# Performance work log

Measured on AMD Instinct MI355X. Metric: run time of the kernel, lower is better.

## Reference

```python
import jax, jax.numpy as jnp
import numpy as np

EPS = 1e-5


def setup_inputs() -> dict:
    key = jax.random.key(0)
    ks = jax.random.split(key, 7)
    N, M, D, H, DM = 8192, 128, 64, 8, 1024  # tokens, num_memories, d_memory, heads, d_model
    return {
        "query": jax.random.normal(ks[0], (N, DM), dtype=jnp.float32),
        "addresses": jax.random.normal(ks[1], (M, D), dtype=jnp.float32),
        "memories": jax.random.normal(ks[2], (N, M, D), dtype=jnp.float32),
        "Wq": jax.random.normal(ks[3], (DM, H * D), dtype=jnp.float32) / np.sqrt(DM),
        "bq": jax.random.normal(ks[4], (H * D,), dtype=jnp.float32) * 0.01,
        "Wo": jax.random.normal(ks[5], (H * D, DM), dtype=jnp.float32) / np.sqrt(H * D),
        "bo": jax.random.normal(ks[6], (DM,), dtype=jnp.float32) * 0.01,
    }


def reference(query, addresses, memories, Wq, bq, Wo, bo):
    N = query.shape[0]
    M, D = addresses.shape
    # Query projection -> heads: (N, H, D)
    q = (query @ Wq + bq).reshape(N, -1, D)
    q = jax.nn.relu(q)  # kernel feature map on query
    # Keys: memory content + learned addresses, kernel feature map
    k = jax.nn.relu(memories + addresses)  # (N, M, D)
    # make_kernel: contract over the num_memories dim
    matrix = jnp.einsum("nmd,nme->nde", k, memories)  # (N, D, D)
    normalizer = jnp.sum(k, axis=-2)  # (N, D)
    # read_from_kernel
    numerator = jnp.einsum("nhd,nde->nhe", q, matrix)  # (N, H, D)
    denominator = jnp.einsum("nhd,nd->nh", q, normalizer)[..., None] + EPS
    attn = numerator / denominator  # (N, H, D)
    # merge heads back to d_model
    return attn.reshape(N, -1) @ Wo + bo
```

## Files before the change

### kernel.cpp

```cpp
#include <hip/hip_runtime.h>

typedef __bf16 bf16x8 __attribute__((ext_vector_type(8)));
typedef __bf16 bf16x4 __attribute__((ext_vector_type(4)));
typedef __bf16 bf16x2 __attribute__((ext_vector_type(2)));
typedef float  f32x4  __attribute__((ext_vector_type(4)));

__device__ __forceinline__ void gload_lds16(const void* g, void* l) {
    auto gp = reinterpret_cast<const __attribute__((address_space(1))) unsigned int*>(
        reinterpret_cast<uintptr_t>(g));
    auto lp = reinterpret_cast<__attribute__((address_space(3))) unsigned int*>(
        reinterpret_cast<uintptr_t>(l));
    __builtin_amdgcn_global_load_lds(gp, lp, 16, 0, 0);
}

__global__ __launch_bounds__(256) void convert_to_bf16(
    const float* __restrict__ src, __bf16* __restrict__ dst, int n8)
{
    const int i = blockIdx.x * 256 + threadIdx.x;
    if (i < n8) {
        f32x4 a = ((const f32x4*)src)[2 * i];
        f32x4 b = ((const f32x4*)src)[2 * i + 1];
        bf16x8 o;
        #pragma unroll
        for (int j = 0; j < 4; ++j) { o[j] = (__bf16)a[j]; o[4 + j] = (__bf16)b[j]; }
        ((bf16x8*)dst)[i] = o;
    }
}

__global__ __launch_bounds__(256) void transpose_to_bf16(
    const float* __restrict__ src, __bf16* __restrict__ dst, int R, int C)
{
    __shared__ float tile[32][33];
    const int tx = threadIdx.x & 31, ty = threadIdx.x >> 5;
    const int r0 = blockIdx.y * 32, c0 = blockIdx.x * 32;
    #pragma unroll
    for (int i = ty; i < 32; i += 8)
        tile[i][tx] = src[(size_t)(r0 + i) * C + c0 + tx];
    __syncthreads();
    #pragma unroll
    for (int i = ty; i < 32; i += 8)
        dst[(size_t)(c0 + i) * R + r0 + tx] = (__bf16)tile[tx][i];
}

template<bool RELU, bool OBF16>
__global__ __launch_bounds__(256) void gemm_lds(
    const __bf16* __restrict__ A, const __bf16* __restrict__ BT,
    const float* __restrict__ bias, void* __restrict__ Outp,
    int M, int N, int K)
{
    __shared__ __bf16 As[128][32];
    __shared__ __bf16 Bs[128][32];

    const int tid = threadIdx.x, lane = tid & 63, w = tid >> 6;
    const int wm = w >> 1, wn = w & 1;
    const int m0 = blockIdx.y * 128, n0 = blockIdx.x * 128;
    const int r = lane & 15, g = lane >> 4;

    const int srow = lane >> 2;
    const int scol = (lane & 3) * 8;
    const __bf16* gA = A  + (size_t)(m0 + 32 * w + srow) * K + scol;
    const __bf16* gB = BT + (size_t)(n0 + 32 * w + srow) * K + scol;

    f32x4 acc[4][4];
    const f32x4 zero = {0.f, 0.f, 0.f, 0.f};
    #pragma unroll
    for (int mi = 0; mi < 4; ++mi)
        #pragma unroll
        for (int ni = 0; ni < 4; ++ni) acc[mi][ni] = zero;

    for (int k0 = 0; k0 < K; k0 += 32) {
        __syncthreads();
        gload_lds16(gA + k0,          &As[32 * w][0]);
        gload_lds16(gA + 16 * K + k0, &As[32 * w + 16][0]);
        gload_lds16(gB + k0,          &Bs[32 * w][0]);
        gload_lds16(gB + 16 * K + k0, &Bs[32 * w + 16][0]);
        __syncthreads();

        bf16x8 af[4], bfr[4];
        #pragma unroll
        for (int mi = 0; mi < 4; ++mi)
            af[mi] = *(const bf16x8*)&As[wm * 64 + mi * 16 + r][g * 8];
        #pragma unroll
        for (int ni = 0; ni < 4; ++ni)
            bfr[ni] = *(const bf16x8*)&Bs[wn * 64 + ni * 16 + r][g * 8];
        #pragma unroll
        for (int mi = 0; mi < 4; ++mi)
            #pragma unroll
            for (int ni = 0; ni < 4; ++ni)
                acc[mi][ni] = __builtin_amdgcn_mfma_f32_16x16x32_bf16(
                    af[mi], bfr[ni], acc[mi][ni], 0, 0, 0);
    }

    const int orow = m0 + wm * 64 + g * 4;
    const int ocol = n0 + wn * 64 + r;
    #pragma unroll
    for (int ni = 0; ni < 4; ++ni) {
        const float bb = bias[ocol + ni * 16];
        #pragma unroll
        for (int mi = 0; mi < 4; ++mi) {
            #pragma unroll
            for (int q = 0; q < 4; ++q) {
                float v = acc[mi][ni][q] + bb;
                if constexpr (RELU) v = fmaxf(v, 0.f);
                const size_t o = (size_t)(orow + mi * 16 + q) * N + ocol + ni * 16;
                if constexpr (OBF16) ((__bf16*)Outp)[o] = (__bf16)v;
                else                 ((float*)Outp)[o]  = v;
            }
        }
    }
}

__device__ __forceinline__ int kbyte(int m, int e) {
    return m * 128 + ((((e >> 3) ^ (m & 7))) << 4) + (e & 7) * 2;
}

__global__ __launch_bounds__(256, 4) void memory_attn_mfma(
    const __bf16* __restrict__ Q,
    const float*  __restrict__ mem,
    const __bf16* __restrict__ adrb,
    __bf16* __restrict__ attn)
{
    __shared__ __align__(16) unsigned char kbuf[4][4096];
    __shared__ __align__(16) unsigned char tbuf[4][5120];
    __shared__ float denl[4][8];

    const int tid = threadIdx.x, lane = tid & 63, w = tid >> 6;
    const int n = blockIdx.x * 4 + w;
    const int v = lane & 15, g = lane >> 4;
    const int e4 = 4 * v;

    unsigned char* kb = kbuf[w];
    unsigned char* tb = tbuf[w];
    const float* pmem = mem + (size_t)n * 128 * 64;

    const __bf16* qp = Q + (size_t)n * 512 + v * 64 + 8 * g;
    const bf16x8 qf0 = *(const bf16x8*)(qp);
    const bf16x8 qf1 = *(const bf16x8*)(qp + 32);

    f32x4 acc[4];
    const f32x4 zero = {0.f, 0.f, 0.f, 0.f};
    #pragma unroll
    for (int nb = 0; nb < 4; ++nb) acc[nb] = zero;
    float psum = 0.f;

    f32x4 cm[8];
    #pragma unroll
    for (int i = 0; i < 4; ++i) {
        const int mo = 8 * i + 2 * g;
        cm[2 * i]     = *(const f32x4*)(pmem + (size_t)mo * 64 + e4);
        cm[2 * i + 1] = *(const f32x4*)(pmem + (size_t)(mo + 1) * 64 + e4);
    }

    #pragma unroll
    for (int c = 0; c < 4; ++c) {
        const int mb = c * 32;
        f32x4 nm[8];
        if (c < 3) {
            #pragma unroll
            for (int i = 0; i < 4; ++i) {
                const int mo = mb + 32 + 8 * i + 2 * g;
                nm[2 * i]     = *(const f32x4*)(pmem + (size_t)mo * 64 + e4);
                nm[2 * i + 1] = *(const f32x4*)(pmem + (size_t)(mo + 1) * 64 + e4);
            }
        }
        #pragma unroll
        for (int i = 0; i < 4; ++i) {
            const int mo = mb + 8 * i + 2 * g;
            const bf16x4 a0 = *(const bf16x4*)(adrb + (size_t)(mo & 127) * 64 + e4);
            const bf16x4 a1 = *(const bf16x4*)(adrb + (size_t)((mo + 1) & 127) * 64 + e4);
            const f32x4 m0 = cm[2 * i], m1 = cm[2 * i + 1];
            bf16x4 k0, k1;
            #pragma unroll
            for (int j = 0; j < 4; ++j) {
                k0[j] = (__bf16)fmaxf(m0[j] + (float)a0[j], 0.f);
                k1[j] = (__bf16)fmaxf(m1[j] + (float)a1[j], 0.f);
            }
            const int mo_l = mo & 31;
            *(bf16x4*)(kb + kbyte(mo_l,     e4)) = k0;
            *(bf16x4*)(kb + kbyte(mo_l + 1, e4)) = k1;
            const int kap = 8 * ((mo_l >> 2) & 3) + 4 * (mo_l >> 4) + (mo_l & 3);
            #pragma unroll
            for (int j2 = 0; j2 < 4; ++j2) {
                bf16x2 p = { (__bf16)m0[j2], (__bf16)m1[j2] };
                *(bf16x2*)(tb + (size_t)(e4 + j2) * 80 + kap * 2) = p;
            }
        }

        f32x4 sA0 = zero, sA1 = zero;
        {
            const bf16x8 a00 = *(const bf16x8*)(kb + kbyte(v,      8 * g));
            const bf16x8 a01 = *(const bf16x8*)(kb + kbyte(v,      32 + 8 * g));
            const bf16x8 a10 = *(const bf16x8*)(kb + kbyte(v + 16, 8 * g));
            const bf16x8 a11 = *(const bf16x8*)(kb + kbyte(v + 16, 32 + 8 * g));
            sA0 = __builtin_amdgcn_mfma_f32_16x16x32_bf16(a00, qf0, sA0, 0, 0, 0);
            sA0 = __builtin_amdgcn_mfma_f32_16x16x32_bf16(a01, qf1, sA0, 0, 0, 0);
            sA1 = __builtin_amdgcn_mfma_f32_16x16x32_bf16(a10, qf0, sA1, 0, 0, 0);
            sA1 = __builtin_amdgcn_mfma_f32_16x16x32_bf16(a11, qf1, sA1, 0, 0, 0);
        }
        psum += sA0[0] + sA0[1] + sA0[2] + sA0[3]
              + sA1[0] + sA1[1] + sA1[2] + sA1[3];

        bf16x8 pa;
        #pragma unroll
        for (int q = 0; q < 4; ++q) {
            pa[q]     = (__bf16)sA0[q];
            pa[4 + q] = (__bf16)sA1[q];
        }

        #pragma unroll
        for (int nb = 0; nb < 4; ++nb) {
            const bf16x8 bf = *(const bf16x8*)(tb + (size_t)(16 * nb + v) * 80 + 16 * g);
            acc[nb] = __builtin_amdgcn_mfma_f32_16x16x32_bf16(pa, bf, acc[nb], 0, 0, 0);
        }

        if (c < 3) {
            #pragma unroll
            for (int t = 0; t < 8; ++t) cm[t] = nm[t];
        }
    }

    psum += __shfl_xor(psum, 16);
    psum += __shfl_xor(psum, 32);
    if (lane < 8) denl[w][lane] = psum;

    if (g < 2) {
        const f32x4 d4 = *(const f32x4*)&denl[w][4 * g];
        float inv[4];
        #pragma unroll
        for (int q = 0; q < 4; ++q) inv[q] = 1.f / (d4[q] + 1e-5f);
        #pragma unroll
        for (int nb = 0; nb < 4; ++nb) {
            #pragma unroll
            for (int q = 0; q < 4; ++q) {
                attn[(size_t)n * 512 + (4 * g + q) * 64 + 16 * nb + v] =
                    (__bf16)(acc[nb][q] * inv[q]);
            }
        }
    }
}

extern "C" void kernel_launch(void* const* d_in, const int* in_sizes, int n_in,
                              void* d_out, int out_size, void* d_ws, size_t ws_size,
                              hipStream_t stream)
{
    const float* query     = (const float*)d_in[0];
    const float* addresses = (const float*)d_in[1];
    const float* memories  = (const float*)d_in[2];
    const float* Wq        = (const float*)d_in[3];
    const float* bq        = (const float*)d_in[4];
    const float* Wo        = (const float*)d_in[5];
    const float* bo        = (const float*)d_in[6];
    float* out = (float*)d_out;

    char* ws = (char*)d_ws;
    __bf16* WqT  = (__bf16*)(ws);
    __bf16* WoT  = (__bf16*)(ws + (1 << 20));
    __bf16* Qb   = (__bf16*)(ws + (2 << 20));
    __bf16* Ab   = (__bf16*)(ws + (10 << 20));
    __bf16* Adrb = (__bf16*)(ws + (18 << 20));
    __bf16* Qbf  = (__bf16*)d_out;

    convert_to_bf16<<<4096, 256, 0, stream>>>(query, Qbf, 8192 * 1024 / 8);
    convert_to_bf16<<<4, 256, 0, stream>>>(addresses, Adrb, 128 * 64 / 8);
    transpose_to_bf16<<<dim3(512 / 32, 1024 / 32), 256, 0, stream>>>(Wq, WqT, 1024, 512);
    transpose_to_bf16<<<dim3(1024 / 32, 512 / 32), 256, 0, stream>>>(Wo, WoT, 512, 1024);

    gemm_lds<true, true><<<dim3(512 / 128, 8192 / 128), 256, 0, stream>>>(
        Qbf, WqT, bq, Qb, 8192, 512, 1024);

    memory_attn_mfma<<<dim3(8192 / 4), 256, 0, stream>>>(Qb, memories, Adrb, Ab);

    gemm_lds<false, false><<<dim3(1024 / 128, 8192 / 128), 256, 0, stream>>>(
        Ab, WoT, bo, out, 8192, 1024, 512);
}
```

Baseline: 128.8 us.

## Retile Q-projection GEMM and remap memory loads in attention kernel

The GEMM gains a BN template parameter, and the query projection now uses 64-wide column tiles. This doubles its block count (256 to 512) so more compute units have work. In the memory-attention kernel, each lane now loads four consecutive memory rows instead of two interleaved pairs, which lets the transposed tile be written as bf16x4 rather than bf16x2. The occupancy hint drops from 4 to 3 blocks per CU, which gives the compiler more registers for the larger per-lane staging. The risks are lower occupancy and more redundant A-tile loads in the smaller-tile GEMM.

```diff
diff --git a/kernel.cpp b/kernel.cpp
--- a/kernel.cpp
+++ b/kernel.cpp
@@ -42,59 +42,61 @@
         dst[(size_t)(c0 + i) * R + r0 + tx] = (__bf16)tile[tx][i];
 }
 
-template<bool RELU, bool OBF16>
+template<int BN, bool RELU, bool OBF16>
 __global__ __launch_bounds__(256) void gemm_lds(
     const __bf16* __restrict__ A, const __bf16* __restrict__ BT,
     const float* __restrict__ bias, void* __restrict__ Outp,
     int M, int N, int K)
 {
+    constexpr int FN = BN / 32;
     __shared__ __bf16 As[128][32];
-    __shared__ __bf16 Bs[128][32];
+    __shared__ __bf16 Bs[BN][32];
 
     const int tid = threadIdx.x, lane = tid & 63, w = tid >> 6;
     const int wm = w >> 1, wn = w & 1;
-    const int m0 = blockIdx.y * 128, n0 = blockIdx.x * 128;
+    const int m0 = blockIdx.y * 128, n0 = blockIdx.x * BN;
     const int r = lane & 15, g = lane >> 4;
 
     const int srow = lane >> 2;
     const int scol = (lane & 3) * 8;
     const __bf16* gA = A  + (size_t)(m0 + 32 * w + srow) * K + scol;
-    const __bf16* gB = BT + (size_t)(n0 + 32 * w + srow) * K + scol;
-
-    f32x4 acc[4][4];
+    const __bf16* gB = BT + (size_t)(n0 + (BN / 4) * w + srow) * K + scol;
+
+    f32x4 acc[4][FN];
     const f32x4 zero = {0.f, 0.f, 0.f, 0.f};
     #pragma unroll
     for (int mi = 0; mi < 4; ++mi)
         #pragma unroll
-        for (int ni = 0; ni < 4; ++ni) acc[mi][ni] = zero;
+        for (int ni = 0; ni < FN; ++ni) acc[mi][ni] = zero;
 
     for (int k0 = 0; k0 < K; k0 += 32) {
         __syncthreads();
         gload_lds16(gA + k0,          &As[32 * w][0]);
         gload_lds16(gA + 16 * K + k0, &As[32 * w + 16][0]);
-        gload_lds16(gB + k0,          &Bs[32 * w][0]);
-        gload_lds16(gB + 16 * K + k0, &Bs[32 * w + 16][0]);
+        #pragma unroll
+        for (int t = 0; t < BN / 64; ++t)
+            gload_lds16(gB + (size_t)(16 * t) * K + k0, &Bs[(BN / 4) * w + 16 * t][0]);
         __syncthreads();
 
-        bf16x8 af[4], bfr[4];
+        bf16x8 af[4], bfr[FN];
         #pragma unroll
         for (int mi = 0; mi < 4; ++mi)
             af[mi] = *(const bf16x8*)&As[wm * 64 + mi * 16 + r][g * 8];
         #pragma unroll
-        for (int ni = 0; ni < 4; ++ni)
-            bfr[ni] = *(const bf16x8*)&Bs[wn * 64 + ni * 16 + r][g * 8];
+        for (int ni = 0; ni < FN; ++ni)
+            bfr[ni] = *(const bf16x8*)&Bs[wn * (FN * 16) + ni * 16 + r][g * 8];
         #pragma unroll
         for (int mi = 0; mi < 4; ++mi)
             #pragma unroll
-            for (int ni = 0; ni < 4; ++ni)
+            for (int ni = 0; ni < FN; ++ni)
                 acc[mi][ni] = __builtin_amdgcn_mfma_f32_16x16x32_bf16(
                     af[mi], bfr[ni], acc[mi][ni], 0, 0, 0);
     }
 
     const int orow = m0 + wm * 64 + g * 4;
-    const int ocol = n0 + wn * 64 + r;
-    #pragma unroll
-    for (int ni = 0; ni < 4; ++ni) {
+    const int ocol = n0 + wn * (FN * 16) + r;
+    #pragma unroll
+    for (int ni = 0; ni < FN; ++ni) {
         const float bb = bias[ocol + ni * 16];
         #pragma unroll
         for (int mi = 0; mi < 4; ++mi) {
@@ -114,7 +116,7 @@
     return m * 128 + ((((e >> 3) ^ (m & 7))) << 4) + (e & 7) * 2;
 }
 
-__global__ __launch_bounds__(256, 4) void memory_attn_mfma(
+__global__ __launch_bounds__(256, 3) void memory_attn_mfma(
     const __bf16* __restrict__ Q,
     const float*  __restrict__ mem,
     const __bf16* __restrict__ adrb,
@@ -127,7 +129,8 @@
     const int tid = threadIdx.x, lane = tid & 63, w = tid >> 6;
     const int n = blockIdx.x * 4 + w;
     const int v = lane & 15, g = lane >> 4;
-    const int e4 = 4 * v;
+    const int sv = lane >> 2, sg = lane & 3;
+    const int e4s = 4 * sv;
 
     unsigned char* kb = kbuf[w];
     unsigned char* tb = tbuf[w];
@@ -145,11 +148,10 @@
 
     f32x4 cm[8];
     #pragma unroll
-    for (int i = 0; i < 4; ++i) {
-        const int mo = 8 * i + 2 * g;
-        cm[2 * i]     = *(const f32x4*)(pmem + (size_t)mo * 64 + e4);
-        cm[2 * i + 1] = *(const f32x4*)(pmem + (size_t)(mo + 1) * 64 + e4);
-    }
+    for (int i = 0; i < 2; ++i)
+        #pragma unroll
+        for (int j = 0; j < 4; ++j)
+            cm[4 * i + j] = *(const f32x4*)(pmem + (size_t)(16 * i + 4 * sg + j) * 64 + e4s);
 
     #pragma unroll
     for (int c = 0; c < 4; ++c) {
@@ -157,32 +159,32 @@
         f32x4 nm[8];
         if (c < 3) {
             #pragma unroll
-            for (int i = 0; i < 4; ++i) {
-                const int mo = mb + 32 + 8 * i + 2 * g;
-                nm[2 * i]     = *(const f32x4*)(pmem + (size_t)mo * 64 + e4);
-                nm[2 * i + 1] = *(const f32x4*)(pmem + (size_t)(mo + 1) * 64 + e4);
-            }
-        }
-        #pragma unroll
-        for (int i = 0; i < 4; ++i) {
-            const int mo = mb + 8 * i + 2 * g;
-            const bf16x4 a0 = *(const bf16x4*)(adrb + (size_t)(mo & 127) * 64 + e4);
-            const bf16x4 a1 = *(const bf16x4*)(adrb + (size_t)((mo + 1) & 127) * 64 + e4);
-            const f32x4 m0 = cm[2 * i], m1 = cm[2 * i + 1];
-            bf16x4 k0, k1;
+            for (int i = 0; i < 2; ++i)
+                #pragma unroll
+                for (int j = 0; j < 4; ++j)
+                    nm[4 * i + j] = *(const f32x4*)(
+                        pmem + (size_t)(mb + 32 + 16 * i + 4 * sg + j) * 64 + e4s);
+        }
+        #pragma unroll
+        for (int i = 0; i < 2; ++i) {
+            const int mo_b = 16 * i + 4 * sg;
             #pragma unroll
             for (int j = 0; j < 4; ++j) {
-                k0[j] = (__bf16)fmaxf(m0[j] + (float)a0[j], 0.f);
-                k1[j] = (__bf16)fmaxf(m1[j] + (float)a1[j], 0.f);
-            }
-            const int mo_l = mo & 31;
-            *(bf16x4*)(kb + kbyte(mo_l,     e4)) = k0;
-            *(bf16x4*)(kb + kbyte(mo_l + 1, e4)) = k1;
-            const int kap = 8 * ((mo_l >> 2) & 3) + 4 * (mo_l >> 4) + (mo_l & 3);
-            #pragma unroll
-            for (int j2 = 0; j2 < 4; ++j2) {
-                bf16x2 p = { (__bf16)m0[j2], (__bf16)m1[j2] };
-                *(bf16x2*)(tb + (size_t)(e4 + j2) * 80 + kap * 2) = p;
+                const int mo = mo_b + j;
+                const bf16x4 av = *(const bf16x4*)(adrb + (size_t)(mb + mo) * 64 + e4s);
+                const f32x4 mv = cm[4 * i + j];
+                bf16x4 kv;
+                #pragma unroll
+                for (int t = 0; t < 4; ++t)
+                    kv[t] = (__bf16)fmaxf(mv[t] + (float)av[t], 0.f);
+                *(bf16x4*)(kb + kbyte(mo, e4s)) = kv;
+            }
+            const int kb2 = 16 * sg + 8 * i;
+            #pragma unroll
+            for (int t = 0; t < 4; ++t) {
+                bf16x4 p = { (__bf16)cm[4 * i + 0][t], (__bf16)cm[4 * i + 1][t],
+                             (__bf16)cm[4 * i + 2][t], (__bf16)cm[4 * i + 3][t] };
+                *(bf16x4*)(tb + (size_t)(e4s + t) * 80 + kb2) = p;
             }
         }
 
@@ -265,11 +267,11 @@
     transpose_to_bf16<<<dim3(512 / 32, 1024 / 32), 256, 0, stream>>>(Wq, WqT, 1024, 512);
     transpose_to_bf16<<<dim3(1024 / 32, 512 / 32), 256, 0, stream>>>(Wo, WoT, 512, 1024);
 
-    gemm_lds<true, true><<<dim3(512 / 128, 8192 / 128), 256, 0, stream>>>(
+    gemm_lds<64, true, true><<<dim3(512 / 64, 8192 / 128), 256, 0, stream>>>(
         Qbf, WqT, bq, Qb, 8192, 512, 1024);
 
     memory_attn_mfma<<<dim3(8192 / 4), 256, 0, stream>>>(Qb, memories, Adrb, Ab);
 
-    gemm_lds<false, false><<<dim3(1024 / 128, 8192 / 128), 256, 0, stream>>>(
+    gemm_lds<128, false, false><<<dim3(1024 / 128, 8192 / 128), 256, 0, stream>>>(
         Ab, WoT, bo, out, 8192, 1024, 512);
 }
```

After: 132.5 us. 1.03x slower.

## Fuse query bf16 conversion into Q-projection GEMM and merge prep kernels

Applied to the files above, without the earlier changes.

Removes the separate pass that converts the full fp32 query matrix to bf16 by having the Q-projection GEMM load fp32 tiles and convert them while staging into LDS, with a narrower 64-column tile to increase block count. The weight transposes and address conversion are merged into one launch to cut launch overhead. The memory-attention kernel drops its software prefetch of memories and its launch bounds, relying on the compiler and occupancy instead. The GEMM's fp32 A loads are now synchronous register loads rather than async LDS loads, and the query is re-read across eight column blocks instead of four.

```diff
diff --git a/kernel.cpp b/kernel.cpp
--- a/kernel.cpp
+++ b/kernel.cpp
@@ -13,39 +13,115 @@
     __builtin_amdgcn_global_load_lds(gp, lp, 16, 0, 0);
 }
 
-__global__ __launch_bounds__(256) void convert_to_bf16(
-    const float* __restrict__ src, __bf16* __restrict__ dst, int n8)
-{
-    const int i = blockIdx.x * 256 + threadIdx.x;
-    if (i < n8) {
-        f32x4 a = ((const f32x4*)src)[2 * i];
-        f32x4 b = ((const f32x4*)src)[2 * i + 1];
+__global__ __launch_bounds__(256) void prep_all(
+    const float* __restrict__ Wq, const float* __restrict__ Wo,
+    const float* __restrict__ adr,
+    __bf16* __restrict__ WqT, __bf16* __restrict__ WoT,
+    __bf16* __restrict__ adrb)
+{
+    __shared__ float tile[32][33];
+    const int bid = blockIdx.x, tid = threadIdx.x;
+
+    if (bid < 1024) {
+        const float* src; __bf16* dst; int R, C, r0, c0;
+        if (bid < 512) {
+            src = Wq; dst = WqT; R = 1024; C = 512;
+            c0 = (bid & 15) * 32; r0 = (bid >> 4) * 32;
+        } else {
+            const int b = bid - 512;
+            src = Wo; dst = WoT; R = 512; C = 1024;
+            c0 = (b & 31) * 32; r0 = (b >> 5) * 32;
+        }
+        const int tx = tid & 31, ty = tid >> 5;
+        #pragma unroll
+        for (int i = ty; i < 32; i += 8)
+            tile[i][tx] = src[(size_t)(r0 + i) * C + c0 + tx];
+        __syncthreads();
+        #pragma unroll
+        for (int i = ty; i < 32; i += 8)
+            dst[(size_t)(c0 + i) * R + r0 + tx] = (__bf16)tile[tx][i];
+    } else {
+        const int i = (bid - 1024) * 256 + tid;
+        f32x4 a = ((const f32x4*)adr)[2 * i];
+        f32x4 b = ((const f32x4*)adr)[2 * i + 1];
         bf16x8 o;
         #pragma unroll
         for (int j = 0; j < 4; ++j) { o[j] = (__bf16)a[j]; o[4 + j] = (__bf16)b[j]; }
-        ((bf16x8*)dst)[i] = o;
-    }
-}
-
-__global__ __launch_bounds__(256) void transpose_to_bf16(
-    const float* __restrict__ src, __bf16* __restrict__ dst, int R, int C)
-{
-    __shared__ float tile[32][33];
-    const int tx = threadIdx.x & 31, ty = threadIdx.x >> 5;
-    const int r0 = blockIdx.y * 32, c0 = blockIdx.x * 32;
-    #pragma unroll
-    for (int i = ty; i < 32; i += 8)
-        tile[i][tx] = src[(size_t)(r0 + i) * C + c0 + tx];
-    __syncthreads();
-    #pragma unroll
-    for (int i = ty; i < 32; i += 8)
-        dst[(size_t)(c0 + i) * R + r0 + tx] = (__bf16)tile[tx][i];
-}
-
-template<bool RELU, bool OBF16>
-__global__ __launch_bounds__(256) void gemm_lds(
+        ((bf16x8*)adrb)[i] = o;
+    }
+}
+
+__global__ __launch_bounds__(256) void gemm_qproj(
+    const float* __restrict__ A, const __bf16* __restrict__ BT,
+    const float* __restrict__ bias, __bf16* __restrict__ Out,
+    int M, int N, int K)
+{
+    __shared__ __bf16 As[128][40];
+    __shared__ __bf16 Bs[64][32];
+
+    const int tid = threadIdx.x, lane = tid & 63, w = tid >> 6;
+    const int wm = w >> 1, wn = w & 1;
+    const int m0 = blockIdx.y * 128, n0 = blockIdx.x * 64;
+    const int r = lane & 15, g = lane >> 4;
+
+    const __bf16* gB = BT + (size_t)(n0 + 16 * w + (lane >> 2)) * K + (lane & 3) * 8;
+
+    f32x4 acc[4][2];
+    const f32x4 zero = {0.f, 0.f, 0.f, 0.f};
+    #pragma unroll
+    for (int mi = 0; mi < 4; ++mi)
+        #pragma unroll
+        for (int ni = 0; ni < 2; ++ni) acc[mi][ni] = zero;
+
+    for (int k0 = 0; k0 < K; k0 += 32) {
+        __syncthreads();
+        gload_lds16(gB + k0, &Bs[16 * w][0]);
+        #pragma unroll
+        for (int i = 0; i < 4; ++i) {
+            const int idx = tid + i * 256;
+            const int row = idx >> 3, c4 = (idx & 7) * 4;
+            f32x4 v = *(const f32x4*)(A + (size_t)(m0 + row) * K + k0 + c4);
+            bf16x4 b;
+            b[0] = (__bf16)v[0]; b[1] = (__bf16)v[1];
+            b[2] = (__bf16)v[2]; b[3] = (__bf16)v[3];
+            *(bf16x4*)&As[row][c4] = b;
+        }
+        __syncthreads();
+
+        bf16x8 af[4], bfr[2];
+        #pragma unroll
+        for (int mi = 0; mi < 4; ++mi)
+            af[mi] = *(const bf16x8*)&As[wm * 64 + mi * 16 + r][g * 8];
+        #pragma unroll
+        for (int ni = 0; ni < 2; ++ni)
+            bfr[ni] = *(const bf16x8*)&Bs[wn * 32 + ni * 16 + r][g * 8];
+        #pragma unroll
+        for (int mi = 0; mi < 4; ++mi)
+            #pragma unroll
+            for (int ni = 0; ni < 2; ++ni)
+                acc[mi][ni] = __builtin_amdgcn_mfma_f32_16x16x32_bf16(
+                    af[mi], bfr[ni], acc[mi][ni], 0, 0, 0);
+    }
+
+    const int orow = m0 + wm * 64 + g * 4;
+    const int ocol = n0 + wn * 32 + r;
+    #pragma unroll
+    for (int ni = 0; ni < 2; ++ni) {
+        const float bb = bias[ocol + ni * 16];
+        #pragma unroll
+        for (int mi = 0; mi < 4; ++mi) {
+            #pragma unroll
+            for (int q = 0; q < 4; ++q) {
+                float v = fmaxf(acc[mi][ni][q] + bb, 0.f);
+                Out[(size_t)(orow + mi * 16 + q) * N + ocol + ni * 16] = (__bf16)v;
+            }
+        }
+    }
+}
+
+__global__ __launch_bounds__(256) void gemm_oproj(
     const __bf16* __restrict__ A, const __bf16* __restrict__ BT,
-    const float* __restrict__ bias, void* __restrict__ Outp,
+    const float* __restrict__ bias, float* __restrict__ Out,
     int M, int N, int K)
 {
     __shared__ __bf16 As[128][32];
@@ -100,11 +176,8 @@
         for (int mi = 0; mi < 4; ++mi) {
             #pragma unroll
             for (int q = 0; q < 4; ++q) {
-                float v = acc[mi][ni][q] + bb;
-                if constexpr (RELU) v = fmaxf(v, 0.f);
-                const size_t o = (size_t)(orow + mi * 16 + q) * N + ocol + ni * 16;
-                if constexpr (OBF16) ((__bf16*)Outp)[o] = (__bf16)v;
-                else                 ((float*)Outp)[o]  = v;
+                Out[(size_t)(orow + mi * 16 + q) * N + ocol + ni * 16]
+                    = acc[mi][ni][q] + bb;
             }
         }
     }
@@ -114,7 +187,7 @@
     return m * 128 + ((((e >> 3) ^ (m & 7))) << 4) + (e & 7) * 2;
 }
 
-__global__ __launch_bounds__(256, 4) void memory_attn_mfma(
+__global__ void memory_attn_mfma(
     const __bf16* __restrict__ Q,
     const float*  __restrict__ mem,
     const __bf16* __restrict__ adrb,
@@ -127,11 +200,9 @@
     const int tid = threadIdx.x, lane = tid & 63, w = tid >> 6;
     const int n = blockIdx.x * 4 + w;
     const int v = lane & 15, g = lane >> 4;
-    const int e4 = 4 * v;
 
     unsigned char* kb = kbuf[w];
     unsigned char* tb = tbuf[w];
-    const float* pmem = mem + (size_t)n * 128 * 64;
 
     const __bf16* qp = Q + (size_t)n * 512 + v * 64 + 8 * g;
     const bf16x8 qf0 = *(const bf16x8*)(qp);
@@ -143,46 +214,30 @@
     for (int nb = 0; nb < 4; ++nb) acc[nb] = zero;
     float psum = 0.f;
 
-    f32x4 cm[8];
-    #pragma unroll
-    for (int i = 0; i < 4; ++i) {
-        const int mo = 8 * i + 2 * g;
-        cm[2 * i]     = *(const f32x4*)(pmem + (size_t)mo * 64 + e4);
-        cm[2 * i + 1] = *(const f32x4*)(pmem + (size_t)(mo + 1) * 64 + e4);
-    }
-
-    #pragma unroll
     for (int c = 0; c < 4; ++c) {
         const int mb = c * 32;
-        f32x4 nm[8];
-        if (c < 3) {
-            #pragma unroll
-            for (int i = 0; i < 4; ++i) {
-                const int mo = mb + 32 + 8 * i + 2 * g;
-                nm[2 * i]     = *(const f32x4*)(pmem + (size_t)mo * 64 + e4);
-                nm[2 * i + 1] = *(const f32x4*)(pmem + (size_t)(mo + 1) * 64 + e4);
-            }
-        }
         #pragma unroll
         for (int i = 0; i < 4; ++i) {
-            const int mo = mb + 8 * i + 2 * g;
-            const bf16x4 a0 = *(const bf16x4*)(adrb + (size_t)(mo & 127) * 64 + e4);
-            const bf16x4 a1 = *(const bf16x4*)(adrb + (size_t)((mo + 1) & 127) * 64 + e4);
-            const f32x4 m0 = cm[2 * i], m1 = cm[2 * i + 1];
+            const int mo = 8 * i + 2 * g;
+            const int e  = 4 * v;
+            const float* pm = mem + (((size_t)n * 128 + mb + mo) * 64 + e);
+            const f32x4 m0 = *(const f32x4*)pm;
+            const f32x4 m1 = *(const f32x4*)(pm + 64);
+            const bf16x4 a0 = *(const bf16x4*)(adrb + (size_t)(mb + mo) * 64 + e);
+            const bf16x4 a1 = *(const bf16x4*)(adrb + (size_t)(mb + mo + 1) * 64 + e);
             bf16x4 k0, k1;
             #pragma unroll
             for (int j = 0; j < 4; ++j) {
                 k0[j] = (__bf16)fmaxf(m0[j] + (float)a0[j], 0.f);
                 k1[j] = (__bf16)fmaxf(m1[j] + (float)a1[j], 0.f);
             }
-            const int mo_l = mo & 31;
-            *(bf16x4*)(kb + kbyte(mo_l,     e4)) = k0;
-            *(bf16x4*)(kb + kbyte(mo_l + 1, e4)) = k1;
-            const int kap = 8 * ((mo_l >> 2) & 3) + 4 * (mo_l >> 4) + (mo_l & 3);
+            *(bf16x4*)(kb + kbyte(mo,     e)) = k0;
+            *(bf16x4*)(kb + kbyte(mo + 1, e)) = k1;
+            const int kap = 8 * ((mo >> 2) & 3) + 4 * (mo >> 4) + (mo & 3);
             #pragma unroll
             for (int j2 = 0; j2 < 4; ++j2) {
                 bf16x2 p = { (__bf16)m0[j2], (__bf16)m1[j2] };
-                *(bf16x2*)(tb + (size_t)(e4 + j2) * 80 + kap * 2) = p;
+                *(bf16x2*)(tb + (size_t)(e + j2) * 80 + kap * 2) = p;
             }
         }
 
@@ -212,11 +267,6 @@
             const bf16x8 bf = *(const bf16x8*)(tb + (size_t)(16 * nb + v) * 80 + 16 * g);
             acc[nb] = __builtin_amdgcn_mfma_f32_16x16x32_bf16(pa, bf, acc[nb], 0, 0, 0);
         }
-
-        if (c < 3) {
-            #pragma unroll
-            for (int t = 0; t < 8; ++t) cm[t] = nm[t];
-        }
     }
 
     psum += __shfl_xor(psum, 16);
@@ -258,18 +308,14 @@
     __bf16* Qb   = (__bf16*)(ws + (2 << 20));
     __bf16* Ab   = (__bf16*)(ws + (10 << 20));
     __bf16* Adrb = (__bf16*)(ws + (18 << 20));
-    __bf16* Qbf  = (__bf16*)d_out;
-
-    convert_to_bf16<<<4096, 256, 0, stream>>>(query, Qbf, 8192 * 1024 / 8);
-    convert_to_bf16<<<4, 256, 0, stream>>>(addresses, Adrb, 128 * 64 / 8);
-    transpose_to_bf16<<<dim3(512 / 32, 1024 / 32), 256, 0, stream>>>(Wq, WqT, 1024, 512);
-    transpose_to_bf16<<<dim3(1024 / 32, 512 / 32), 256, 0, stream>>>(Wo, WoT, 512, 1024);
-
-    gemm_lds<true, true><<<dim3(512 / 128, 8192 / 128), 256, 0, stream>>>(
-        Qbf, WqT, bq, Qb, 8192, 512, 1024);
+
+    prep_all<<<1028, 256, 0, stream>>>(Wq, Wo, addresses, WqT, WoT, Adrb);
+
+    gemm_qproj<<<dim3(512 / 64, 8192 / 128), 256, 0, stream>>>(
+        query, WqT, bq, Qb, 8192, 512, 1024);
 
     memory_attn_mfma<<<dim3(8192 / 4), 256, 0, stream>>>(Qb, memories, Adrb, Ab);
 
-    gemm_lds<false, false><<<dim3(1024 / 128, 8192 / 128), 256, 0, stream>>>(
+    gemm_oproj<<<dim3(1024 / 128, 8192 / 128), 256, 0, stream>>>(
         Ab, WoT, bo, out, 8192, 1024, 512);
 }
```

Result: faster. 126.2 us (-2.1%).
